# Kernel tuning notes

Hardware: AMD Instinct MI355X
Metric: run time of the kernel (lower is better)

## Reference

```python
import jax, jax.numpy as jnp
import numpy as np

CP_LEN = 256
FFT_SIZE = 1024
OFFSET = CP_LEN // 2                      # 128
PILOT_SPACING = 100
NSYMS = 824
TOTAL_SYMS = NSYMS + 1 + NSYMS // PILOT_SPACING   # 833
PAD_L = (FFT_SIZE - TOTAL_SYMS) // 2      # 95
PAD_R = FFT_SIZE - PAD_L - TOTAL_SYMS     # 96
PILOTS_IDX = np.arange(PAD_L, FFT_SIZE - PAD_R, PILOT_SPACING)  # 9 pilots

def _data_indices():
    # Statically unroll the original while-loop: gather all non-pilot data bins.
    idxs = []
    idx = 0
    jj = PAD_L + 1
    while idx < NSYMS:
        n = min(PILOT_SPACING - 1, NSYMS - idx)
        idxs.extend(range(jj, jj + n))
        idx += n
        jj += n + 1
    return np.asarray(idxs, dtype=np.int32)

DATA_IDX = _data_indices()  # [824]


def setup_inputs() -> dict:
    key = jax.random.key(0)
    # [batch, n_symbols, 2*(FFT_SIZE+CP_LEN)] interleaved I/Q floats
    in1 = jax.random.normal(key, (16, 1024, 2 * (FFT_SIZE + CP_LEN)), dtype=jnp.float32)
    return {"in1": in1}


def reference(in1):
    t = jnp.arange(FFT_SIZE, dtype=jnp.float32)
    # Deinterleave I/Q -> complex64
    iq = jax.lax.complex(in1[:, :, ::2], in1[:, :, 1::2])
    # FFT of the window starting at half the CP, then fftshift via roll
    spec = jnp.fft.fft(iq[:, :, OFFSET:OFFSET + FFT_SIZE], axis=2)
    result = jnp.roll(spec, FFT_SIZE // 2, axis=2)
    # Compensate timing-offset phase ramp
    result = result * jnp.exp(1j * OFFSET * t * (2.0 * np.pi / FFT_SIZE))
    # Estimate residual slope from pilot phase differences (wrapped to [-pi,pi])
    a = jnp.diff(jnp.angle(result[:, :, PILOTS_IDX]), axis=2)
    a = jnp.where(a > np.pi, a - 2.0 * np.pi, a)
    a = jnp.where(a < -np.pi, a + 2.0 * np.pi, a)
    mn = jnp.mean(a, axis=2)  # [B, S]
    result = result * jnp.exp(-1j * t * mn[:, :, None] / PILOT_SPACING)
    # Gather data (non-pilot) bins and interleave real/imag -> [B, S, 2*NSYMS]
    data = result[:, :, DATA_IDX]
    x = jnp.stack([data.real, data.imag], axis=-1).reshape(
        data.shape[0], data.shape[1], 2 * NSYMS)
    return x.astype(jnp.float32)
```

## Files before the change

kernel.cpp:

```cpp
#include <hip/hip_runtime.h>
#include <math.h>

#define NT      256
#define NSYMS   824
#define NPILOT  9

#define PADIDX(k) ((k) + ((k) >> 4))

#define C32_TWOPI_1024  6.1359233222901821136474609375e-3f

__device__ __forceinline__ float2 cmulf(float2 a, float2 b) {
    return make_float2(a.x * b.x - a.y * b.y, a.x * b.y + a.y * b.x);
}

template <int T2>
__device__ __forceinline__ void r4_stage(const float2* __restrict__ src,
                                         float2* __restrict__ dst,
                                         const float2* __restrict__ W,
                                         int i) {
    const int s = 1 << T2;
    const int r = i & (s - 1);
    const int p = i & ~(s - 1);
    const int pb = PADIDX(i);
    float2 a = src[pb];
    float2 b = src[pb + 272];
    float2 c = src[pb + 544];
    float2 d = src[pb + 816];
    float2 w1 = W[PADIDX(p)];
    float2 w2 = W[PADIDX(2 * p)];
    float2 w3 = W[PADIDX(3 * p)];
    float2 t0  = make_float2(a.x + c.x, a.y + c.y);
    float2 t1  = make_float2(a.x - c.x, a.y - c.y);
    float2 t2c = make_float2(b.x + d.x, b.y + d.y);
    float2 t3  = make_float2(b.x - d.x, b.y - d.y);
    float2 y0  = make_float2(t0.x + t2c.x, t0.y + t2c.y);
    float2 e1  = make_float2(t1.x + t3.y, t1.y - t3.x);
    float2 e2  = make_float2(t0.x - t2c.x, t0.y - t2c.y);
    float2 e3  = make_float2(t1.x - t3.y, t1.y + t3.x);
    const int j0 = ((i >> T2) << (T2 + 2)) | r;
    dst[PADIDX(j0)]         = y0;
    dst[PADIDX(j0 + s)]     = cmulf(w1, e1);
    dst[PADIDX(j0 + 2 * s)] = cmulf(w2, e2);
    dst[PADIDX(j0 + 3 * s)] = cmulf(w3, e3);
}

__global__ __launch_bounds__(NT, 5) void ofdm_kernel(const float* __restrict__ in,
                                                     float* __restrict__ out) {
    __shared__ double2 T256[256];
    __shared__ double2 u_s[NT];
    __shared__ float2  bufA[1088];
    __shared__ float2  bufB[1088];
    __shared__ float2  W[816];
    __shared__ double  ang[NPILOT];

    const int row = blockIdx.x;
    const int tid = threadIdx.x;

    const float2* rin2 = (const float2*)(in + (size_t)row * 2560) + 128;
    float2 v0 = rin2[tid];
    float2 v1 = rin2[tid + 256];
    float2 v2 = rin2[tid + 512];
    float2 v3 = rin2[tid + 768];

    double ux = ((double)v0.x - (double)v2.x) - ((double)v1.y - (double)v3.y);
    double uy = ((double)v0.y - (double)v2.y) + ((double)v1.x - (double)v3.x);

    {
        double sn, cs;
        sincos((double)tid * -6.1359231515425649189e-3, &sn, &cs);
        T256[tid] = make_double2(cs, sn);
        float cf = (float)cs, sf = (float)sn;
        W[PADIDX(tid)]       = make_float2(cf, sf);
        W[PADIDX(tid + 256)] = make_float2(sf, -cf);
        W[PADIDX(tid + 512)] = make_float2(-cf, -sf);
    }

    bufA[PADIDX(tid)]       = v0;
    bufA[PADIDX(tid + 256)] = v1;
    bufA[PADIDX(tid + 512)] = v2;
    bufA[PADIDX(tid + 768)] = v3;
    u_s[tid] = make_double2(ux, uy);
    __syncthreads();

    if (tid < 16 * NPILOT) {
        const int p  = tid >> 4;
        const int g  = tid & 15;
        const int jj = 95 + 100 * p;
        const int K  = (jj + 512) & 1023;
        int idx = (K * g) & 1023;
        const int step = (K * 16) & 1023;
        double2 acc = make_double2(0.0, 0.0);
        #pragma unroll
        for (int m = 0; m < 16; m++) {
            double2 uu = u_s[g + 16 * m];
            double2 w  = T256[idx & 255];
            const int q = idx >> 8;
            double wx = w.x, wy = w.y;
            if (q & 1) { double t = wx; wx = wy; wy = -t; }
            if (q & 2) { wx = -wx; wy = -wy; }
            acc.x += wx * uu.x - wy * uu.y;
            acc.y += wx * uu.y + wy * uu.x;
            idx = (idx + step) & 1023;
        }
        #pragma unroll
        for (int off = 1; off < 16; off <<= 1) {
            acc.x += __shfl_xor(acc.x, off, 64);
            acc.y += __shfl_xor(acc.y, off, 64);
        }
        if (g == 0) {
            float th32 = (float)(128 * jj) * C32_TWOPI_1024;
            double sn, cs;
            sincos((double)th32, &sn, &cs);
            double csf = (double)(float)cs;
            double snf = (double)(float)sn;
            double re = acc.x * csf - acc.y * snf;
            double im = acc.x * snf + acc.y * csf;
            ang[p] = atan2(im, re);
        }
    }
    r4_stage<0>(bufA, bufB, W, tid);
    __syncthreads();
    r4_stage<2>(bufB, bufA, W, tid);
    __syncthreads();
    r4_stage<4>(bufA, bufB, W, tid);
    __syncthreads();
    r4_stage<6>(bufB, bufA, W, tid);
    __syncthreads();

    double mn;
    {
        double sum = 0.0;
        double prev = ang[0];
        #pragma unroll
        for (int k = 1; k < NPILOT; k++) {
            double cur = ang[k];
            double a = cur - prev;
            if (a > 3.14159265358979323846)       a -= 6.28318530717958647693;
            else if (a < -3.14159265358979323846) a += 6.28318530717958647693;
            sum += a;
            prev = cur;
        }
        mn = sum * 0.125;
    }

    {
        const int pb = PADIDX(tid);
        float2 a = bufA[pb];
        float2 b = bufA[pb + 272];
        float2 c = bufA[pb + 544];
        float2 d = bufA[pb + 816];
        float2 t0  = make_float2(a.x + c.x, a.y + c.y);
        float2 t1  = make_float2(a.x - c.x, a.y - c.y);
        float2 t2c = make_float2(b.x + d.x, b.y + d.y);
        float2 t3  = make_float2(b.x - d.x, b.y - d.y);
        float2 y0  = make_float2(t0.x + t2c.x, t0.y + t2c.y);
        float2 y1  = make_float2(t1.x + t3.y, t1.y - t3.x);
        float2 y2  = make_float2(t0.x - t2c.x, t0.y - t2c.y);
        float2 y3  = make_float2(t1.x - t3.y, t1.y + t3.x);

        float2* rout = (float2*)(out + (size_t)row * (2 * NSYMS));
        float2 ys[4] = { y2, y3, y0, y1 };
        #pragma unroll
        for (int k = 0; k < 4; k++) {
            const int jj = tid + 256 * k;
            if (jj >= 96 && jj <= 927 && ((jj - 95) % 100) != 0) {
                const int dd = jj - 96 - (jj - 96) / 100;
                float2 z = ys[k];
                float th32 = (float)(128 * jj) * C32_TWOPI_1024;
                float ph = th32 - (float)(mn * 0.01 * (double)jj);
                float sn, cs;
                __sincosf(ph, &sn, &cs);
                rout[dd] = make_float2(z.x * cs - z.y * sn,
                                       z.x * sn + z.y * cs);
            }
        }
    }
}

extern "C" void kernel_launch(void* const* d_in, const int* in_sizes, int n_in,
                              void* d_out, int out_size, void* d_ws, size_t ws_size,
                              hipStream_t stream) {
    const float* in = (const float*)d_in[0];
    float* out = (float*)d_out;
    ofdm_kernel<<<dim3(16 * 1024), dim3(NT), 0, stream>>>(in, out);
}
```

Baseline: 294.6 us.

## Switch FFT to in-place DIF with single buffer and precomputed twiddle tables

Replaces the out-of-place Stockham radix-4 stages, which ping-pong between two buffers, with in-place decimation-in-frequency stages on one shared buffer. The final stage now reads bit-reversed (digit-reversed) positions. Twiddles are reduced to a 256-entry table with quadrant rotation, and the sincos table is computed once by a separate init kernel into workspace rather than per block. Together these cut LDS use and per-block transcendental work, so launch bounds rise to 8 blocks per CU. The cost is an extra tiny kernel launch and scattered, digit-reversed output indexing that may make the global writes less coalesced.

```diff
diff --git a/kernel.cpp b/kernel.cpp
--- a/kernel.cpp
+++ b/kernel.cpp
@@ -13,44 +13,58 @@
     return make_float2(a.x * b.x - a.y * b.y, a.x * b.y + a.y * b.x);
 }
 
-template <int T2>
-__device__ __forceinline__ void r4_stage(const float2* __restrict__ src,
-                                         float2* __restrict__ dst,
-                                         const float2* __restrict__ W,
-                                         int i) {
-    const int s = 1 << T2;
-    const int r = i & (s - 1);
-    const int p = i & ~(s - 1);
-    const int pb = PADIDX(i);
-    float2 a = src[pb];
-    float2 b = src[pb + 272];
-    float2 c = src[pb + 544];
-    float2 d = src[pb + 816];
-    float2 w1 = W[PADIDX(p)];
-    float2 w2 = W[PADIDX(2 * p)];
-    float2 w3 = W[PADIDX(3 * p)];
-    float2 t0  = make_float2(a.x + c.x, a.y + c.y);
-    float2 t1  = make_float2(a.x - c.x, a.y - c.y);
-    float2 t2c = make_float2(b.x + d.x, b.y + d.y);
-    float2 t3  = make_float2(b.x - d.x, b.y - d.y);
-    float2 y0  = make_float2(t0.x + t2c.x, t0.y + t2c.y);
-    float2 e1  = make_float2(t1.x + t3.y, t1.y - t3.x);
-    float2 e2  = make_float2(t0.x - t2c.x, t0.y - t2c.y);
-    float2 e3  = make_float2(t1.x - t3.y, t1.y + t3.x);
-    const int j0 = ((i >> T2) << (T2 + 2)) | r;
-    dst[PADIDX(j0)]         = y0;
-    dst[PADIDX(j0 + s)]     = cmulf(w1, e1);
-    dst[PADIDX(j0 + 2 * s)] = cmulf(w2, e2);
-    dst[PADIDX(j0 + 3 * s)] = cmulf(w3, e3);
+template <int LM, int F>
+__device__ __forceinline__ void dif_stage(float2* __restrict__ buf,
+                                          const float2* __restrict__ W256,
+                                          int i) {
+    const int r = i & (LM - 1);
+    const int base = ((i & ~(LM - 1)) << 2) | r;
+    float2 a = buf[PADIDX(base)];
+    float2 b = buf[PADIDX(base + LM)];
+    float2 c = buf[PADIDX(base + 2 * LM)];
+    float2 d = buf[PADIDX(base + 3 * LM)];
+    float2 t0 = make_float2(a.x + c.x, a.y + c.y);
+    float2 t1 = make_float2(a.x - c.x, a.y - c.y);
+    float2 t2 = make_float2(b.x + d.x, b.y + d.y);
+    float2 t3 = make_float2(b.x - d.x, b.y - d.y);
+    float2 y0 = make_float2(t0.x + t2.x, t0.y + t2.y);
+    float2 y1 = make_float2(t1.x + t3.y, t1.y - t3.x);
+    float2 y2 = make_float2(t0.x - t2.x, t0.y - t2.y);
+    float2 y3 = make_float2(t1.x - t3.y, t1.y + t3.x);
+    const int e1 = F * r;
+    const int e2 = 2 * F * r;
+    const int e3 = 3 * F * r;
+    float2 w1 = W256[PADIDX(e1)];
+    float2 w2 = W256[PADIDX(e2 & 255)];
+    if (e2 & 256) w2 = make_float2(w2.y, -w2.x);
+    float2 w3 = W256[PADIDX(e3 & 255)];
+    {
+        const int q = e3 >> 8;
+        if (q == 1)      w3 = make_float2(w3.y, -w3.x);
+        else if (q == 2) w3 = make_float2(-w3.x, -w3.y);
+    }
+    buf[PADIDX(base)]          = y0;
+    buf[PADIDX(base + LM)]     = cmulf(w1, y1);
+    buf[PADIDX(base + 2 * LM)] = cmulf(w2, y2);
+    buf[PADIDX(base + 3 * LM)] = cmulf(w3, y3);
 }
 
-__global__ __launch_bounds__(NT, 5) void ofdm_kernel(const float* __restrict__ in,
-                                                     float* __restrict__ out) {
+__global__ void table_init(double2* __restrict__ Tg, float2* __restrict__ Wg) {
+    const int t = threadIdx.x;
+    double sn, cs;
+    sincos((double)t * -6.1359231515425649189e-3, &sn, &cs);
+    Tg[t] = make_double2(cs, sn);
+    Wg[t] = make_float2((float)cs, (float)sn);
+}
+
+__global__ __launch_bounds__(NT, 8) void ofdm_kernel(const float* __restrict__ in,
+                                                     float* __restrict__ out,
+                                                     const double2* __restrict__ Tg,
+                                                     const float2* __restrict__ Wg) {
     __shared__ double2 T256[256];
     __shared__ double2 u_s[NT];
-    __shared__ float2  bufA[1088];
-    __shared__ float2  bufB[1088];
-    __shared__ float2  W[816];
+    __shared__ float2  buf[1088];
+    __shared__ float2  W256[272];
     __shared__ double  ang[NPILOT];
 
     const int row = blockIdx.x;
@@ -62,23 +76,16 @@
     float2 v2 = rin2[tid + 512];
     float2 v3 = rin2[tid + 768];
 
+    T256[tid] = Tg[tid];
+    W256[PADIDX(tid)] = Wg[tid];
+
     double ux = ((double)v0.x - (double)v2.x) - ((double)v1.y - (double)v3.y);
     double uy = ((double)v0.y - (double)v2.y) + ((double)v1.x - (double)v3.x);
 
-    {
-        double sn, cs;
-        sincos((double)tid * -6.1359231515425649189e-3, &sn, &cs);
-        T256[tid] = make_double2(cs, sn);
-        float cf = (float)cs, sf = (float)sn;
-        W[PADIDX(tid)]       = make_float2(cf, sf);
-        W[PADIDX(tid + 256)] = make_float2(sf, -cf);
-        W[PADIDX(tid + 512)] = make_float2(-cf, -sf);
-    }
-
-    bufA[PADIDX(tid)]       = v0;
-    bufA[PADIDX(tid + 256)] = v1;
-    bufA[PADIDX(tid + 512)] = v2;
-    bufA[PADIDX(tid + 768)] = v3;
+    buf[PADIDX(tid)]       = v0;
+    buf[PADIDX(tid + 256)] = v1;
+    buf[PADIDX(tid + 512)] = v2;
+    buf[PADIDX(tid + 768)] = v3;
     u_s[tid] = make_double2(ux, uy);
     __syncthreads();
 
@@ -118,13 +125,13 @@
             ang[p] = atan2(im, re);
         }
     }
-    r4_stage<0>(bufA, bufB, W, tid);
+    dif_stage<256, 1>(buf, W256, tid);
     __syncthreads();
-    r4_stage<2>(bufB, bufA, W, tid);
+    dif_stage<64, 4>(buf, W256, tid);
     __syncthreads();
-    r4_stage<4>(bufA, bufB, W, tid);
+    dif_stage<16, 16>(buf, W256, tid);
     __syncthreads();
-    r4_stage<6>(bufB, bufA, W, tid);
+    dif_stage<4, 64>(buf, W256, tid);
     __syncthreads();
 
     double mn;
@@ -144,25 +151,28 @@
     }
 
     {
-        const int pb = PADIDX(tid);
-        float2 a = bufA[pb];
-        float2 b = bufA[pb + 272];
-        float2 c = bufA[pb + 544];
-        float2 d = bufA[pb + 816];
-        float2 t0  = make_float2(a.x + c.x, a.y + c.y);
-        float2 t1  = make_float2(a.x - c.x, a.y - c.y);
-        float2 t2c = make_float2(b.x + d.x, b.y + d.y);
-        float2 t3  = make_float2(b.x - d.x, b.y - d.y);
-        float2 y0  = make_float2(t0.x + t2c.x, t0.y + t2c.y);
-        float2 y1  = make_float2(t1.x + t3.y, t1.y - t3.x);
-        float2 y2  = make_float2(t0.x - t2c.x, t0.y - t2c.y);
-        float2 y3  = make_float2(t1.x - t3.y, t1.y + t3.x);
+        const int pb = PADIDX(4 * tid);
+        float2 a = buf[pb];
+        float2 b = buf[pb + 1];
+        float2 c = buf[pb + 2];
+        float2 d = buf[pb + 3];
+        float2 t0 = make_float2(a.x + c.x, a.y + c.y);
+        float2 t1 = make_float2(a.x - c.x, a.y - c.y);
+        float2 t2 = make_float2(b.x + d.x, b.y + d.y);
+        float2 t3 = make_float2(b.x - d.x, b.y - d.y);
+        float2 y0 = make_float2(t0.x + t2.x, t0.y + t2.y);
+        float2 y1 = make_float2(t1.x + t3.y, t1.y - t3.x);
+        float2 y2 = make_float2(t0.x - t2.x, t0.y - t2.y);
+        float2 y3 = make_float2(t1.x - t3.y, t1.y + t3.x);
+
+        const int R = ((tid & 3) << 6) | (((tid >> 2) & 3) << 4) |
+                      (((tid >> 4) & 3) << 2) | ((tid >> 6) & 3);
 
         float2* rout = (float2*)(out + (size_t)row * (2 * NSYMS));
         float2 ys[4] = { y2, y3, y0, y1 };
         #pragma unroll
         for (int k = 0; k < 4; k++) {
-            const int jj = tid + 256 * k;
+            const int jj = R + 256 * k;
             if (jj >= 96 && jj <= 927 && ((jj - 95) % 100) != 0) {
                 const int dd = jj - 96 - (jj - 96) / 100;
                 float2 z = ys[k];
@@ -182,5 +192,8 @@
                               hipStream_t stream) {
     const float* in = (const float*)d_in[0];
     float* out = (float*)d_out;
-    ofdm_kernel<<<dim3(16 * 1024), dim3(NT), 0, stream>>>(in, out);
+    double2* Tg = (double2*)d_ws;
+    float2*  Wg = (float2*)((char*)d_ws + 4096);
+    table_init<<<dim3(1), dim3(256), 0, stream>>>(Tg, Wg);
+    ofdm_kernel<<<dim3(16 * 1024), dim3(NT), 0, stream>>>(in, out, Tg, Wg);
 }
```

Measured after the change: 281.5 us. 4.4% less time.
